# Performance work log

Hardware: AMD Instinct MI355X
Metric: run time of the kernel (lower is better)

## Reference

```python
import jax, jax.numpy as jnp
import numpy as np

N_NODES = 100000
N_EDGES = 1600000
IN_FEATS = 128
N_HIDDEN = 128
N_CLASSES = 64


def setup_inputs() -> dict:
    key = jax.random.key(0)
    ks = jax.random.split(key, 12)
    features = jax.random.normal(ks[0], (N_NODES, IN_FEATS), dtype=jnp.float32)
    src = jax.random.randint(ks[1], (N_EDGES,), 0, N_NODES, dtype=jnp.int32)
    dst = jax.random.randint(ks[2], (N_EDGES,), 0, N_NODES, dtype=jnp.int32)
    def lin(k, fi, fo):
        s = 1.0 / np.sqrt(fi)
        kw, kb = jax.random.split(k)
        W = jax.random.uniform(kw, (fi, fo), jnp.float32, -s, s)
        b = jax.random.uniform(kb, (fo,), jnp.float32, -s, s)
        return W, b
    W1, b1 = lin(ks[3], IN_FEATS, N_HIDDEN)
    W2a, b2a = lin(ks[4], N_HIDDEN, N_HIDDEN)
    W2b, b2b = lin(ks[5], N_HIDDEN, N_HIDDEN)
    W3, b3 = lin(ks[6], N_HIDDEN, N_CLASSES)
    eps = jnp.zeros((4,), jnp.float32)  # learnable eps, one per GINConv
    return dict(features=features, src=src, dst=dst, W1=W1, b1=b1,
                W2a=W2a, b2a=b2a, W2b=W2b, b2b=b2b, W3=W3, b3=b3, eps=eps)


def _aggregate(h, src, dst, mode, deg):
    # messages flow src -> dst; h[src] is [E, d]
    msg = h[src]
    if mode == 'sum':
        return jax.ops.segment_sum(msg, dst, num_segments=N_NODES)
    if mode == 'mean':
        s = jax.ops.segment_sum(msg, dst, num_segments=N_NODES)
        return s / jnp.maximum(deg, 1.0)[:, None]
    # max: DGL yields 0 for nodes with no incoming edges
    m = jax.ops.segment_max(msg, dst, num_segments=N_NODES)
    return jnp.where(deg[:, None] > 0, m, 0.0)


def reference(features, src, dst, W1, b1, W2a, b2a, W2b, b2b, W3, b3, eps):
    deg = jax.ops.segment_sum(jnp.ones((N_EDGES,), jnp.float32), dst,
                              num_segments=N_NODES)
    h = features
    # layer 0: max aggregation + Linear + ReLU (dropout = identity in eval)
    h = (1.0 + eps[0]) * h + _aggregate(h, src, dst, 'max', deg)
    h = jax.nn.relu(h @ W1 + b1)
    # middle layers: sum aggregation + Linear + ReLU
    h = (1.0 + eps[1]) * h + _aggregate(h, src, dst, 'sum', deg)
    h = jax.nn.relu(h @ W2a + b2a)
    h = (1.0 + eps[2]) * h + _aggregate(h, src, dst, 'sum', deg)
    h = jax.nn.relu(h @ W2b + b2b)
    # output layer: mean aggregation + Linear (no activation)
    h = (1.0 + eps[3]) * h + _aggregate(h, src, dst, 'mean', deg)
    h = h @ W3 + b3
    return h
```

## Files before the change

### kernel.cpp

```cpp
#include <hip/hip_runtime.h>
#include <math.h>

#define N_NODES 100000
#define N_EDGES 1600000
#define FEAT 128
#define NBUCKET 391
#define BCAP 5120

typedef __attribute__((ext_vector_type(8))) _Float16 half8;
typedef __attribute__((ext_vector_type(4))) float floatx4;

__device__ inline half8 h8max(half8 a, half8 b) {
    return __builtin_elementwise_max(a, b);
}

__global__ __launch_bounds__(256) void zero_i32(int* p, int n) {
    int i = blockIdx.x * 256 + threadIdx.x;
    if (i < n) p[i] = 0;
}

__global__ __launch_bounds__(512) void bin_edges(const int* __restrict__ src,
                                                 const int* __restrict__ dst,
                                                 uint2* __restrict__ ebuf,
                                                 int* __restrict__ gcur) {
    __shared__ int hist[NBUCKET];
    __shared__ int lbase[NBUCKET];
    __shared__ int cur[NBUCKET];
    __shared__ uint2 tile[4096];

    int t = threadIdx.x;
    int e0 = blockIdx.x * 4096;
    for (int i = t; i < NBUCKET; i += 512) { hist[i] = 0; cur[i] = 0; }
    __syncthreads();

    for (int i = t; i < 4096; i += 512) {
        int e = e0 + i;
        uint2 v; v.x = 0u; v.y = 0xffffffffu;
        if (e < N_EDGES) { v.x = (unsigned)src[e]; v.y = (unsigned)dst[e]; }
        tile[i] = v;
        if (v.y != 0xffffffffu) atomicAdd(&hist[v.y >> 8], 1);
    }
    __syncthreads();

    for (int i = t; i < NBUCKET; i += 512) {
        int c = hist[i];
        lbase[i] = (c > 0) ? atomicAdd(&gcur[i], c) : 0;
    }
    __syncthreads();

    for (int i = t; i < 4096; i += 512) {
        uint2 v = tile[i];
        if (v.y == 0xffffffffu) continue;
        int b = (int)(v.y >> 8);
        int p = lbase[b] + atomicAdd(&cur[b], 1);
        if (p < BCAP) ebuf[(size_t)b * BCAP + p] = v;
    }
}

__global__ __launch_bounds__(512) void scan_buckets(const int* __restrict__ gcur,
                                                    int* __restrict__ bbase,
                                                    int* __restrict__ rowptr) {
    __shared__ int s[512];
    int t = threadIdx.x;
    int v = (t < NBUCKET) ? gcur[t] : 0;
    s[t] = v;
    __syncthreads();
    for (int off = 1; off < 512; off <<= 1) {
        int u = (t >= off) ? s[t - off] : 0;
        __syncthreads();
        s[t] += u;
        __syncthreads();
    }
    if (t < NBUCKET) bbase[t] = s[t] - v;
    if (t == 0) rowptr[N_NODES] = N_EDGES;
}

__global__ __launch_bounds__(256) void bucket_csr(const uint2* __restrict__ ebuf,
                                                  const int* __restrict__ gcur,
                                                  const int* __restrict__ bbase,
                                                  int* __restrict__ rowptr,
                                                  int* __restrict__ esrc) {
    __shared__ int cnt[256];
    __shared__ int off[256];
    __shared__ int astart[256];
    __shared__ int cur[256];

    int b = blockIdx.x, t = threadIdx.x;
    int total = gcur[b]; if (total > BCAP) total = BCAP;
    int base = bbase[b];
    const uint2* eb = ebuf + (size_t)b * BCAP;

    cnt[t] = 0; cur[t] = 0;
    __syncthreads();
    for (int i = t; i < total; i += 256) atomicAdd(&cnt[eb[i].y & 255], 1);
    __syncthreads();

    int v = cnt[t];
    off[t] = v;
    __syncthreads();
    for (int o = 1; o < 256; o <<= 1) {
        int u = (t >= o) ? off[t - o] : 0;
        __syncthreads();
        off[t] += u;
        __syncthreads();
    }
    int excl = off[t] - v;
    int node = (b << 8) + t;
    if (node < N_NODES) rowptr[node] = base + excl;
    astart[t] = base + excl;
    __syncthreads();

    for (int i = t; i < total; i += 256) {
        uint2 e = eb[i];
        int ln = (int)(e.y & 255);
        int p = astart[ln] + atomicAdd(&cur[ln], 1);
        esrc[p] = (int)e.x;
    }
}

__global__ __launch_bounds__(256) void f32_to_f16_vec(const float* __restrict__ in,
                                                      _Float16* __restrict__ out,
                                                      int n4) {
    int i = blockIdx.x * 256 + threadIdx.x;
    int stride = gridDim.x * 256;
    for (; i < n4; i += stride) {
        float4 v = ((const float4*)in)[i];
        union { uint2 u; _Float16 h[4]; } p;
        p.h[0] = (_Float16)v.x; p.h[1] = (_Float16)v.y;
        p.h[2] = (_Float16)v.z; p.h[3] = (_Float16)v.w;
        *(uint2*)(out + 4 * (size_t)i) = p.u;
    }
}

__global__ __launch_bounds__(256) void wprep(const float* __restrict__ W,
                                             _Float16* __restrict__ WT,
                                             int K, int N) {
    int idx = blockIdx.x * 256 + threadIdx.x;
    if (idx < K * N) {
        int n = idx / K, k = idx % K;
        WT[idx] = (_Float16)W[k * N + n];
    }
}

template <int MODE, int D, bool OUTF32, bool BIAS>
__global__ __launch_bounds__(256) void agg_kernel(const _Float16* __restrict__ h,
                                                  const int* __restrict__ rowptr,
                                                  const int* __restrict__ esrc,
                                                  const float* __restrict__ eps,
                                                  int ei,
                                                  const float* __restrict__ bias,
                                                  _Float16* __restrict__ outH,
                                                  float* __restrict__ outF) {
    constexpr int LPE = D / 8;
    constexpr int NG = 64 / LPE;
    int node = (int)((blockIdx.x * 256 + threadIdx.x) >> 6);
    if (node >= N_NODES) return;
    int l = threadIdx.x & 63;
    int grp = l / LPE, sl = l & (LPE - 1);
    int beg = rowptr[node], end = rowptr[node + 1];
    int deg = end - beg;

    _Float16 init = (MODE == 0) ? (_Float16)(-65504.0f) : (_Float16)(0.0f);
    half8 acc = {init, init, init, init, init, init, init, init};

    int e = beg;
    for (; e + 2 * NG <= end; e += 2 * NG) {
        int s0 = esrc[e + grp];
        int s1 = esrc[e + NG + grp];
        half8 v0 = *(const half8*)(h + (size_t)s0 * D + sl * 8);
        half8 v1 = *(const half8*)(h + (size_t)s1 * D + sl * 8);
        if (MODE == 0) acc = h8max(acc, h8max(v0, v1));
        else           acc += v0 + v1;
    }
    for (; e < end; e += NG) {
        int ee = e + grp;
        if (ee < end) {
            int s = esrc[ee];
            half8 v = *(const half8*)(h + (size_t)s * D + sl * 8);
            if (MODE == 0) acc = h8max(acc, v);
            else           acc += v;
        }
    }

    union HU { half8 h; int w[4]; };
    HU U; U.h = acc;
#pragma unroll
    for (int m = LPE; m < 64; m <<= 1) {
        HU V;
#pragma unroll
        for (int k = 0; k < 4; ++k) V.w[k] = __shfl_xor(U.w[k], m, 64);
        if (MODE == 0) U.h = h8max(U.h, V.h);
        else           U.h = U.h + V.h;
    }

    if (grp != 0) return;

    float a[8];
#pragma unroll
    for (int i = 0; i < 8; ++i) a[i] = (float)U.h[i];
    if (MODE == 0 && deg == 0) {
#pragma unroll
        for (int i = 0; i < 8; ++i) a[i] = 0.f;
    }
    if (MODE == 2) {
        float inv = 1.f / (float)(deg > 0 ? deg : 1);
#pragma unroll
        for (int i = 0; i < 8; ++i) a[i] *= inv;
    }
    float sc = 1.f + eps[ei];
    half8 self = *(const half8*)(h + (size_t)node * D + sl * 8);
    float o[8];
#pragma unroll
    for (int i = 0; i < 8; ++i) o[i] = fmaf(sc, (float)self[i], a[i]);

    if (OUTF32) {
#pragma unroll
        for (int i = 0; i < 8; ++i)
            if (BIAS) o[i] += bias[sl * 8 + i];
        float4* dstp = (float4*)(outF + (size_t)node * D + sl * 8);
        dstp[0] = make_float4(o[0], o[1], o[2], o[3]);
        dstp[1] = make_float4(o[4], o[5], o[6], o[7]);
    } else {
        half8 ov;
#pragma unroll
        for (int i = 0; i < 8; ++i) ov[i] = (_Float16)o[i];
        *(half8*)(outH + (size_t)node * D + sl * 8) = ov;
    }
}

template <int BN, bool RELU, bool BIAS>
__global__ __launch_bounds__(256) void gemm_mfma(const _Float16* __restrict__ X,
                                                 const _Float16* __restrict__ WT,
                                                 const float* __restrict__ bias,
                                                 _Float16* __restrict__ Yh) {
    __shared__ _Float16 Xs[64 * 128];
    __shared__ _Float16 Ws[BN * 128];
    char* xb = (char*)Xs;
    char* wb = (char*)Ws;

    int t = threadIdx.x;
    int l = t & 63, w = t >> 6;
    int lr = l & 15, lg = l >> 4;
    int rowBase = blockIdx.x * 64;

    {
        int row = t >> 2, q = t & 3;
        int grow = rowBase + row;
        const char* srcp = (const char*)(X + (size_t)grow * 128) + q * 64;
#pragma unroll
        for (int j = 0; j < 4; ++j) {
            int byte = q * 64 + j * 16;
            half8 v = {};
            if (grow < N_NODES) v = *(const half8*)(srcp + j * 16);
            *(half8*)(xb + row * 256 + (byte ^ ((row & 7) << 4))) = v;
        }
    }
    {
#pragma unroll
        for (int p = 0; p < BN / 16; ++p) {
            int idx = p * 4096 + t * 16;
            int row = idx >> 8, byte = idx & 255;
            *(half8*)(wb + row * 256 + (byte ^ ((row & 7) << 4))) =
                *(const half8*)((const char*)WT + idx);
        }
    }
    __syncthreads();

    constexpr int NCT = BN / 16;
    floatx4 acc[NCT];
#pragma unroll
    for (int ct = 0; ct < NCT; ++ct)
#pragma unroll
        for (int r = 0; r < 4; ++r) acc[ct][r] = 0.f;

#pragma unroll
    for (int ks = 0; ks < 4; ++ks) {
        int kbyte = ks * 64 + lg * 16;
        int r = w * 16 + lr;
        half8 a = *(const half8*)(xb + r * 256 + (kbyte ^ ((r & 7) << 4)));
#pragma unroll
        for (int ct = 0; ct < NCT; ++ct) {
            int n = ct * 16 + lr;
            half8 b = *(const half8*)(wb + n * 256 + (kbyte ^ ((n & 7) << 4)));
            acc[ct] = __builtin_amdgcn_mfma_f32_16x16x32_f16(a, b, acc[ct], 0, 0, 0);
        }
    }

    float bv[NCT];
#pragma unroll
    for (int ct = 0; ct < NCT; ++ct) bv[ct] = BIAS ? bias[ct * 16 + lr] : 0.f;

    constexpr int ROWB = BN * 2;
    __syncthreads();
#pragma unroll
    for (int ct = 0; ct < NCT; ++ct)
#pragma unroll
        for (int r = 0; r < 4; ++r) {
            int row = w * 16 + lg * 4 + r;
            int col = ct * 16 + lr;
            float v = acc[ct][r] + bv[ct];
            if (RELU) v = fmaxf(v, 0.f);
            *(_Float16*)(xb + row * ROWB + ((col * 2) ^ ((row & 7) << 4))) =
                (_Float16)v;
        }
    __syncthreads();
    {
        int row = t >> 2, q = t & 3;
        int grow = rowBase + row;
        if (grow < N_NODES) {
            char* dstp = (char*)(Yh + (size_t)grow * BN) + q * (ROWB / 4);
#pragma unroll
            for (int j = 0; j < ROWB / 64; ++j) {
                int byte = q * (ROWB / 4) + j * 16;
                half8 v = *(const half8*)(xb + row * ROWB + (byte ^ ((row & 7) << 4)));
                *(half8*)(dstp + j * 16) = v;
            }
        }
    }
}

extern "C" void kernel_launch(void* const* d_in, const int* in_sizes, int n_in,
                              void* d_out, int out_size, void* d_ws, size_t ws_size,
                              hipStream_t stream) {
    const float* feat = (const float*)d_in[0];
    const int*   src  = (const int*)d_in[1];
    const int*   dst  = (const int*)d_in[2];
    const float* W1   = (const float*)d_in[3];
    const float* b1   = (const float*)d_in[4];
    const float* W2a  = (const float*)d_in[5];
    const float* b2a  = (const float*)d_in[6];
    const float* W2b  = (const float*)d_in[7];
    const float* b2b  = (const float*)d_in[8];
    const float* W3   = (const float*)d_in[9];
    const float* b3   = (const float*)d_in[10];
    const float* eps  = (const float*)d_in[11];

    const size_t NH = (size_t)N_NODES * FEAT;
    char* base = (char*)d_ws;
    auto alloc = [&](size_t bytes) {
        char* p = base;
        base += (bytes + 255) & ~(size_t)255;
        return p;
    };
    _Float16* featH = (_Float16*)alloc(NH * 2);
    _Float16* hA    = (_Float16*)alloc(NH * 2);
    _Float16* hB    = (_Float16*)alloc(NH * 2);
    _Float16* WT1   = (_Float16*)alloc(128 * 128 * 2);
    _Float16* WT2a  = (_Float16*)alloc(128 * 128 * 2);
    _Float16* WT2b  = (_Float16*)alloc(128 * 128 * 2);
    _Float16* WT3   = (_Float16*)alloc(128 * 64 * 2);
    uint2* ebuf     = (uint2*)alloc((size_t)NBUCKET * BCAP * 8);
    int* rowptr     = (int*)alloc((N_NODES + 1) * 4);
    int* esrc       = (int*)alloc((size_t)N_EDGES * 4);
    int* gcur       = (int*)alloc(NBUCKET * 4);
    int* bbase      = (int*)alloc(NBUCKET * 4);

    f32_to_f16_vec<<<2048, 256, 0, stream>>>(feat, featH, (int)(NH / 4));
    wprep<<<64, 256, 0, stream>>>(W1, WT1, 128, 128);
    wprep<<<64, 256, 0, stream>>>(W2a, WT2a, 128, 128);
    wprep<<<64, 256, 0, stream>>>(W2b, WT2b, 128, 128);
    wprep<<<32, 256, 0, stream>>>(W3, WT3, 128, 64);

    zero_i32<<<(NBUCKET + 255) / 256, 256, 0, stream>>>(gcur, NBUCKET);
    bin_edges<<<(N_EDGES + 4095) / 4096, 512, 0, stream>>>(src, dst, ebuf, gcur);
    scan_buckets<<<1, 512, 0, stream>>>(gcur, bbase, rowptr);
    bucket_csr<<<NBUCKET, 256, 0, stream>>>(ebuf, gcur, bbase, rowptr, esrc);

    const int AGG_GRID = (N_NODES * 64 + 255) / 256;
    const int GEMM_GRID = (N_NODES + 63) / 64;

    agg_kernel<0, 128, false, false><<<AGG_GRID, 256, 0, stream>>>(
        featH, rowptr, esrc, eps, 0, nullptr, hB, nullptr);
    gemm_mfma<128, true, true><<<GEMM_GRID, 256, 0, stream>>>(hB, WT1, b1, hA);
    agg_kernel<1, 128, false, false><<<AGG_GRID, 256, 0, stream>>>(
        hA, rowptr, esrc, eps, 1, nullptr, hB, nullptr);
    gemm_mfma<128, true, true><<<GEMM_GRID, 256, 0, stream>>>(hB, WT2a, b2a, hA);
    agg_kernel<1, 128, false, false><<<AGG_GRID, 256, 0, stream>>>(
        hA, rowptr, esrc, eps, 2, nullptr, hB, nullptr);
    gemm_mfma<128, true, true><<<GEMM_GRID, 256, 0, stream>>>(hB, WT2b, b2b, hA);
    gemm_mfma<64, false, false><<<GEMM_GRID, 256, 0, stream>>>(hA, WT3, nullptr, hB);
    agg_kernel<2, 64, true, true><<<AGG_GRID, 256, 0, stream>>>(
        hB, rowptr, esrc, eps, 3, b3, nullptr, (float*)d_out);
}
```

Before: 358.8 us.

## Assign one node per lane group in aggregation, dropping cross-lane reductions

The aggregation kernel now maps each group of D/8 lanes to its own node, so a wavefront handles 4 (D=128) or 8 (D=64) nodes instead of spreading one node's edges across the whole wave. This removes the shuffle-based cross-group reduction and the idle lanes in the epilogue. Each lane walks its node's edges serially in batches of 8 gathers, clamping and masking the tail to keep more loads in flight. Grid sizes are recomputed to match. In exchange, lanes within a wave now diverge on nodes with different degrees, and the per-edge gather order changes the fp16 summation order.

Result: faster. 342.1 us (-4.7%).

```diff
diff --git a/kernel.cpp b/kernel.cpp
--- a/kernel.cpp
+++ b/kernel.cpp
@@ -152,52 +152,44 @@
                                                   _Float16* __restrict__ outH,
                                                   float* __restrict__ outF) {
     constexpr int LPE = D / 8;
-    constexpr int NG = 64 / LPE;
-    int node = (int)((blockIdx.x * 256 + threadIdx.x) >> 6);
+    constexpr int NPW = 64 / LPE;
+    int wid = (int)((blockIdx.x * 256 + threadIdx.x) >> 6);
+    int l = threadIdx.x & 63;
+    int grp = l / LPE, sl = l % LPE;
+    int node = wid * NPW + grp;
     if (node >= N_NODES) return;
-    int l = threadIdx.x & 63;
-    int grp = l / LPE, sl = l & (LPE - 1);
     int beg = rowptr[node], end = rowptr[node + 1];
     int deg = end - beg;
 
-    _Float16 init = (MODE == 0) ? (_Float16)(-65504.0f) : (_Float16)(0.0f);
-    half8 acc = {init, init, init, init, init, init, init, init};
-
-    int e = beg;
-    for (; e + 2 * NG <= end; e += 2 * NG) {
-        int s0 = esrc[e + grp];
-        int s1 = esrc[e + NG + grp];
-        half8 v0 = *(const half8*)(h + (size_t)s0 * D + sl * 8);
-        half8 v1 = *(const half8*)(h + (size_t)s1 * D + sl * 8);
-        if (MODE == 0) acc = h8max(acc, h8max(v0, v1));
-        else           acc += v0 + v1;
-    }
-    for (; e < end; e += NG) {
-        int ee = e + grp;
-        if (ee < end) {
-            int s = esrc[ee];
-            half8 v = *(const half8*)(h + (size_t)s * D + sl * 8);
-            if (MODE == 0) acc = h8max(acc, v);
-            else           acc += v;
-        }
-    }
-
-    union HU { half8 h; int w[4]; };
-    HU U; U.h = acc;
-#pragma unroll
-    for (int m = LPE; m < 64; m <<= 1) {
-        HU V;
-#pragma unroll
-        for (int k = 0; k < 4; ++k) V.w[k] = __shfl_xor(U.w[k], m, 64);
-        if (MODE == 0) U.h = h8max(U.h, V.h);
-        else           U.h = U.h + V.h;
-    }
-
-    if (grp != 0) return;
+    const _Float16 NEUT = (MODE == 0) ? (_Float16)(-65504.0f) : (_Float16)(0.0f);
+    half8 neut8 = {NEUT, NEUT, NEUT, NEUT, NEUT, NEUT, NEUT, NEUT};
+    half8 acc = neut8;
+
+    for (int e = beg; e < end; e += 8) {
+        half8 v[8];
+#pragma unroll
+        for (int j = 0; j < 8; ++j) {
+            int ee = e + j;
+            int s = esrc[ee < end ? ee : end - 1];
+            v[j] = *(const half8*)(h + (size_t)s * D + sl * 8);
+        }
+#pragma unroll
+        for (int j = 0; j < 8; ++j)
+            if (e + j >= end) v[j] = neut8;
+        if (MODE == 0) {
+            half8 m01 = h8max(v[0], v[1]), m23 = h8max(v[2], v[3]);
+            half8 m45 = h8max(v[4], v[5]), m67 = h8max(v[6], v[7]);
+            acc = h8max(acc, h8max(h8max(m01, m23), h8max(m45, m67)));
+        } else {
+            half8 s01 = v[0] + v[1], s23 = v[2] + v[3];
+            half8 s45 = v[4] + v[5], s67 = v[6] + v[7];
+            acc += (s01 + s23) + (s45 + s67);
+        }
+    }
 
     float a[8];
 #pragma unroll
-    for (int i = 0; i < 8; ++i) a[i] = (float)U.h[i];
+    for (int i = 0; i < 8; ++i) a[i] = (float)acc[i];
     if (MODE == 0 && deg == 0) {
 #pragma unroll
         for (int i = 0; i < 8; ++i) a[i] = 0.f;
@@ -366,19 +358,20 @@
     scan_buckets<<<1, 512, 0, stream>>>(gcur, bbase, rowptr);
     bucket_csr<<<NBUCKET, 256, 0, stream>>>(ebuf, gcur, bbase, rowptr, esrc);
 
-    const int AGG_GRID = (N_NODES * 64 + 255) / 256;
+    const int AGG128_GRID = (N_NODES + 15) / 16;
+    const int AGG64_GRID  = (N_NODES + 31) / 32;
     const int GEMM_GRID = (N_NODES + 63) / 64;
 
-    agg_kernel<0, 128, false, false><<<AGG_GRID, 256, 0, stream>>>(
+    agg_kernel<0, 128, false, false><<<AGG128_GRID, 256, 0, stream>>>(
         featH, rowptr, esrc, eps, 0, nullptr, hB, nullptr);
     gemm_mfma<128, true, true><<<GEMM_GRID, 256, 0, stream>>>(hB, WT1, b1, hA);
-    agg_kernel<1, 128, false, false><<<AGG_GRID, 256, 0, stream>>>(
+    agg_kernel<1, 128, false, false><<<AGG128_GRID, 256, 0, stream>>>(
         hA, rowptr, esrc, eps, 1, nullptr, hB, nullptr);
     gemm_mfma<128, true, true><<<GEMM_GRID, 256, 0, stream>>>(hB, WT2a, b2a, hA);
-    agg_kernel<1, 128, false, false><<<AGG_GRID, 256, 0, stream>>>(
+    agg_kernel<1, 128, false, false><<<AGG128_GRID, 256, 0, stream>>>(
         hA, rowptr, esrc, eps, 2, nullptr, hB, nullptr);
     gemm_mfma<128, true, true><<<GEMM_GRID, 256, 0, stream>>>(hB, WT2b, b2b, hA);
     gemm_mfma<64, false, false><<<GEMM_GRID, 256, 0, stream>>>(hA, WT3, nullptr, hB);
-    agg_kernel<2, 64, true, true><<<AGG_GRID, 256, 0, stream>>>(
+    agg_kernel<2, 64, true, true><<<AGG64_GRID, 256, 0, stream>>>(
         hB, rowptr, esrc, eps, 3, b3, nullptr, (float*)d_out);
 }
```
